# Optimization experiments

Measured on AMD Instinct MI355X. Metric: run time of the kernel, lower is better.

## Reference

```python
import jax, jax.numpy as jnp
import numpy as np

D_MODEL = 256
D_IN = (D_MODEL + 1) ** 2  # 66049


def setup_inputs() -> dict:
    key = jax.random.key(0)
    k1, k2, k3, k4 = jax.random.split(key, 4)
    X = jax.random.normal(k1, (16, 256, 256), dtype=jnp.float32)
    X_aux = jax.random.normal(k2, (16, 256, 256), dtype=jnp.float32)
    # nn.Linear params: weight [out, in], bias [out]
    W = jax.random.normal(k3, (D_MODEL, D_IN), dtype=jnp.float32) / np.sqrt(D_IN)
    b = jax.random.normal(k4, (D_MODEL,), dtype=jnp.float32) * 0.01
    return {"X": X, "X_aux": X_aux, "W": W, "b": b}


def reference(X, X_aux, W, b):
    bsz, t, d = X.shape
    ones = jnp.ones((bsz, t, 1), dtype=X.dtype)
    Xa = jnp.concatenate([ones, X], axis=2)        # [b, t, d+1]
    Xb = jnp.concatenate([ones, X_aux], axis=2)    # [b, t, d+1]
    # outer product per (b, t): [b, t, d+1, d+1]
    tf = jnp.einsum("bti,btj->btij", Xa, Xb)
    tf = tf.reshape(bsz, t, -1)                    # [b, t, (d+1)^2]
    out = jnp.einsum("btk,ok->bto", tf, W) + b     # [b, t, d_model]
    return out
```

## Files before the change

### kernel.cpp

```cpp
#include <hip/hip_runtime.h>
#include <hip/hip_bf16.h>


#define DI 66049

typedef __attribute__((ext_vector_type(8))) short bf16x8;
typedef __attribute__((ext_vector_type(4))) float f32x4;

__device__ __forceinline__ unsigned short f2b(float f) {
  union { __hip_bfloat16 h; unsigned short u; } cv;
  cv.h = __float2bfloat16(f);
  return cv.u;
}

__device__ __forceinline__ bf16x8 pack8(f32x4 lo, f32x4 hi) {
  bf16x8 r;
  r[0] = (short)f2b(lo[0]); r[1] = (short)f2b(lo[1]);
  r[2] = (short)f2b(lo[2]); r[3] = (short)f2b(lo[3]);
  r[4] = (short)f2b(hi[0]); r[5] = (short)f2b(hi[1]);
  r[6] = (short)f2b(hi[2]); r[7] = (short)f2b(hi[3]);
  return r;
}

__device__ __forceinline__ void gload16(const void* g, void* l) {
  __builtin_amdgcn_global_load_lds(
      (const __attribute__((address_space(1))) unsigned int*)g,
      (__attribute__((address_space(3))) unsigned int*)l, 16, 0, 0);
}

__global__ void prep_w(const float* __restrict__ W, unsigned short* __restrict__ Bp) {
  const int c = blockIdx.x;
  const int o = (blockIdx.y << 2) + (threadIdx.x >> 6);
  const int j = (threadIdx.x & 63) << 2;
  const float* wrow = W + (size_t)o * DI;
  float v0, v1, v2, v3;
  if (c < 256) {
    const int bse = (c + 1) * 257 + 1 + j;
    v0 = wrow[bse]; v1 = wrow[bse + 1]; v2 = wrow[bse + 2]; v3 = wrow[bse + 3];
  } else if (c == 256) {
    const int bse = 1 + j;
    v0 = wrow[bse]; v1 = wrow[bse + 1]; v2 = wrow[bse + 2]; v3 = wrow[bse + 3];
  } else {
    v0 = wrow[(j + 1) * 257]; v1 = wrow[(j + 2) * 257];
    v2 = wrow[(j + 3) * 257]; v3 = wrow[(j + 4) * 257];
  }
  unsigned short* dst = Bp + (((size_t)c << 8) + o) * 256 + j;
  const unsigned int lo = (unsigned int)f2b(v0) | ((unsigned int)f2b(v1) << 16);
  const unsigned int hi = (unsigned int)f2b(v2) | ((unsigned int)f2b(v3) << 16);
  *(uint2*)dst = make_uint2(lo, hi);
}

__global__ void prep_xt(const float* __restrict__ X, float* __restrict__ Xt) {
  __shared__ float t[32][33];
  const int tx = threadIdx.x, ty = threadIdx.y;
  const int bt0 = blockIdx.x << 5, c0 = blockIdx.y << 5;
#pragma unroll
  for (int k = 0; k < 4; ++k) {
    const int row = (ty << 2) + k;
    t[row][tx] = X[(size_t)(bt0 + row) * 256 + c0 + tx];
  }
  __syncthreads();
#pragma unroll
  for (int k = 0; k < 4; ++k) {
    const int row = (ty << 2) + k;
    Xt[(size_t)(c0 + row) * 4096 + bt0 + tx] = t[tx][row];
  }
}

#define PACK_AS(SRC)                                                           \
  {                                                                            \
    const int _row = tid >> 2, _q = tid & 3;                                   \
    const float* _rp = (SRC) + (size_t)(bt0 + _row) * 256 + (_q << 6);         \
    const int _sx = _row & 15;                                                 \
    _Pragma("unroll") for (int _w = 0; _w < 8; ++_w) {                         \
      f32x4 _lo = *(const f32x4*)(_rp + (_w << 3));                            \
      f32x4 _hi = *(const f32x4*)(_rp + (_w << 3) + 4);                        \
      const int _slot = (_q << 3) + _w;                                        \
      *(bf16x8*)(&As[_row * 256 + ((_slot ^ _sx) << 3)]) = pack8(_lo, _hi);    \
    }                                                                          \
  }

#define STAGE_U(V, SLOT)                                                       \
  {                                                                            \
    const unsigned short* _bse =                                               \
        Bp + ((size_t)(c0 + ((V) >> 3)) << 16) + (((V) & 7) << 5);             \
    gload16(_bse + stg_off0, &Bs[SLOT][(size_t)tid << 3]);                     \
    gload16(_bse + stg_off1, &Bs[SLOT][(size_t)(512 + tid) << 3]);             \
  }

#define READ_FRAGS(U, S)                                                       \
  {                                                                            \
    const int _uh4 = ((U) & 7) << 2;                                           \
    _Pragma("unroll") for (int _rg = 0; _rg < 4; ++_rg) {                      \
      const int _ra = wr + (_rg << 4) + l15;                                   \
      fa[S][_rg] = *(const bf16x8*)(&As[_ra * 256 +                            \
                                        (((_uh4 + lg) ^ (_ra & 15)) << 3)]);   \
    }                                                                          \
    _Pragma("unroll") for (int _fn = 0; _fn < 4; ++_fn) {                      \
      const int _rb = (wn << 6) + (_fn << 4) + l15;                            \
      fb[S][_fn] = *(const bf16x8*)(&Bs[(U) & 3][_rb * 32 +                    \
                                        ((lg ^ ((_rb >> 1) & 3)) << 3)]);      \
    }                                                                          \
  }

__global__ __launch_bounds__(512, 1) void gemm_r10(
    const float* __restrict__ X, const float* __restrict__ Xb,
    const float* __restrict__ Xt, const unsigned short* __restrict__ Bp,
    float* __restrict__ P) {
  __shared__ __align__(16) unsigned short As[128 * 256];
  __shared__ __align__(16) unsigned short Bs[4][256 * 32];
  __shared__ __align__(16) float Ss[33 * 128];

  const int tid = threadIdx.x;
  const int rid = blockIdx.x;

  int bx, c0, nCh, Pslice;
  const float* Asrc;
  if (rid < 256) {
    const int slice = rid & 7;
    bx = rid >> 3;
    c0 = slice << 5;
    nCh = (slice == 7) ? 33 : 32;
    Asrc = Xb;
    Pslice = slice;
  } else {
    bx = rid - 256;
    c0 = 257;
    nCh = 1;
    Asrc = X;
    Pslice = 8;
  }
  const int bt0 = bx << 7;
  const int nU = nCh << 3;

  const int wid = tid >> 6, lane = tid & 63;
  const int wm = wid >> 2, wn = wid & 3;
  const int wr = wm << 6;
  const int l15 = lane & 15, lg = lane >> 4;

  const int idx0 = tid, idx1 = 512 + tid;
  const int row0 = idx0 >> 2, row1 = idx1 >> 2;
  const unsigned stg_off0 =
      (unsigned)(row0 * 256 + (((idx0 & 3) ^ ((row0 >> 1) & 3)) << 3));
  const unsigned stg_off1 =
      (unsigned)(row1 * 256 + (((idx1 & 3) ^ ((row1 >> 1) & 3)) << 3));

  PACK_AS(Asrc);
  for (int i = tid; i < (nCh << 7); i += 512) {
    const int ci2 = i >> 7, r = i & 127;
    const int c = c0 + ci2;
    Ss[i] = (c < 256) ? Xt[(size_t)c * 4096 + bt0 + r] : 1.0f;
  }
  STAGE_U(0, 0);
  STAGE_U(1, 1);
  STAGE_U(2, 2);
  __syncthreads();

  bf16x8 fa[2][4], fb[2][4];
  READ_FRAGS(0, 0);

  f32x4 acc[4][4] = {};

  for (int ci = 0; ci < nCh; ++ci) {
    f32x4 t[4][4] = {};
    f32x4 s4[4];
#pragma unroll
    for (int uh = 0; uh < 8; ++uh) {
      const int u = (ci << 3) + uh;
      int v = u + 3;
      if (v > nU - 1) v = nU - 1;
      STAGE_U(v, (u + 3) & 3);
      asm volatile("s_waitcnt vmcnt(4)" ::: "memory");
      __builtin_amdgcn_s_barrier();
      int un = u + 1;
      if (un > nU - 1) un = nU - 1;
      if (uh & 1) {
        READ_FRAGS(un, 0);
      } else {
        READ_FRAGS(un, 1);
      }
      if (uh == 7) {
#pragma unroll
        for (int rg = 0; rg < 4; ++rg)
          s4[rg] =
              *(const f32x4*)(&Ss[(ci << 7) + wr + (rg << 4) + (lg << 2)]);
      }
      __builtin_amdgcn_s_setprio(1);
#pragma unroll
      for (int rg = 0; rg < 4; ++rg)
#pragma unroll
        for (int fn = 0; fn < 4; ++fn)
          t[rg][fn] = (uh & 1)
                          ? __builtin_amdgcn_mfma_f32_16x16x32_bf16(
                                fa[1][rg], fb[1][fn], t[rg][fn], 0, 0, 0)
                          : __builtin_amdgcn_mfma_f32_16x16x32_bf16(
                                fa[0][rg], fb[0][fn], t[rg][fn], 0, 0, 0);
      __builtin_amdgcn_s_setprio(0);
    }
#pragma unroll
    for (int rg = 0; rg < 4; ++rg)
#pragma unroll
      for (int fn = 0; fn < 4; ++fn) acc[rg][fn] += s4[rg] * t[rg][fn];
  }

  float* pp = P + ((size_t)Pslice << 20);
#pragma unroll
  for (int rg = 0; rg < 4; ++rg) {
    const int row = bt0 + wr + (rg << 4) + (lg << 2);
#pragma unroll
    for (int fn = 0; fn < 4; ++fn) {
      const int col = (wn << 6) + (fn << 4) + l15;
#pragma unroll
      for (int e = 0; e < 4; ++e)
        pp[(size_t)(row + e) * 256 + col] = acc[rg][fn][e];
    }
  }
}

__global__ void reduce_k(const float* __restrict__ P, const float* __restrict__ W,
                         const float* __restrict__ b, float* __restrict__ out,
                         int nsl) {
  const int idx = blockIdx.x * 256 + threadIdx.x;
  const int o = idx & 255;
  float v = b[o] + W[(size_t)o * DI];
  for (int s = 0; s < nsl; ++s) v += P[idx + (size_t)s * 1048576];
  out[idx] = v;
}

__global__ void init_k(const float* __restrict__ W, const float* __restrict__ b,
                       float* __restrict__ out) {
  const int idx = blockIdx.x * 256 + threadIdx.x;
  const int o = idx & 255;
  out[idx] = b[o] + W[(size_t)o * DI];
}

__global__ __launch_bounds__(256, 4) void gemm_fb(
    const float* __restrict__ X, const float* __restrict__ Xa,
    const float* __restrict__ W, float* __restrict__ Out) {
  __shared__ __align__(16) unsigned short Asf[128 * 64];
  __shared__ __align__(16) unsigned short Bsf[128 * 64];
  const int tid = threadIdx.x;
  const int bx = blockIdx.x, by = blockIdx.y, bz = blockIdx.z;
  const int S = gridDim.z;
  const int bt0 = bx << 7, o0 = by << 7;
  const int q = 258 / S, r = 258 % S;
  const int c0 = bz * q + (bz < r ? bz : r);
  const int ccnt = q + (bz < r ? 1 : 0);
  const int nK = ccnt << 2;
  const int wid = tid >> 6, lane = tid & 63;
  const int wr = (wid >> 1) << 6, wc = (wid & 1) << 6;
  const int ar = tid >> 1;
  const int ah = (tid & 1) << 5;
  const float* xrow = X + (size_t)(bt0 + ar) * 256;
  const float* varow = Xa + (size_t)(bt0 + ar) * 256;
  f32x4 acc[4][4] = {};
  for (int kt = 0; kt < nK; ++kt) {
    const int c = c0 + (kt >> 2);
    const int j0 = (kt & 3) << 6;
    __syncthreads();
    {
      const float* vs = (c == 257) ? xrow : varow;
      float s = 1.0f;
      if (c < 256) s = xrow[c];
      const f32x4* vp = (const f32x4*)(vs + j0 + ah);
      f32x4 v[8];
#pragma unroll
      for (int qq = 0; qq < 8; ++qq) v[qq] = vp[qq];
      unsigned short* aw = Asf + ar * 64;
      const int sl0 = ah >> 3, sx = ar & 7;
#pragma unroll
      for (int w = 0; w < 4; ++w) {
        bf16x8 pk;
#pragma unroll
        for (int e = 0; e < 8; ++e)
          pk[e] = (short)f2b(s * v[w * 2 + (e >> 2)][e & 3]);
        *(bf16x8*)(aw + (((sl0 + w) ^ sx) << 3)) = pk;
      }
    }
    {
      const int orow = tid >> 1;
      const int jh = (tid & 1) << 5;
      const float* wrow = W + (size_t)(o0 + orow) * DI;
      float tmp[32];
      if (c < 256) {
        const int bse = (c + 1) * 257 + 1 + j0 + jh;
#pragma unroll
        for (int i = 0; i < 32; ++i) tmp[i] = wrow[bse + i];
      } else if (c == 256) {
        const int bse = 1 + j0 + jh;
#pragma unroll
        for (int i = 0; i < 32; ++i) tmp[i] = wrow[bse + i];
      } else {
#pragma unroll
        for (int i = 0; i < 32; ++i) tmp[i] = wrow[(j0 + jh + i + 1) * 257];
      }
      unsigned short* bw = Bsf + orow * 64;
      const int sl0 = jh >> 3, sx = orow & 7;
#pragma unroll
      for (int w = 0; w < 4; ++w) {
        bf16x8 pk;
#pragma unroll
        for (int e = 0; e < 8; ++e) pk[e] = (short)f2b(tmp[w * 8 + e]);
        *(bf16x8*)(bw + (((sl0 + w) ^ sx) << 3)) = pk;
      }
    }
    __syncthreads();
#pragma unroll
    for (int kk = 0; kk < 2; ++kk) {
      const int kslot = (kk << 2) + (lane >> 4);
      bf16x8 af[4], bfr2[4];
#pragma unroll
      for (int fm = 0; fm < 4; ++fm) {
        const int row = wr + (fm << 4) + (lane & 15);
        af[fm] = *(const bf16x8*)(Asf + row * 64 + ((kslot ^ (row & 7)) << 3));
      }
#pragma unroll
      for (int fn = 0; fn < 4; ++fn) {
        const int row = wc + (fn << 4) + (lane & 15);
        bfr2[fn] = *(const bf16x8*)(Bsf + row * 64 + ((kslot ^ (row & 7)) << 3));
      }
#pragma unroll
      for (int fm = 0; fm < 4; ++fm)
#pragma unroll
        for (int fn = 0; fn < 4; ++fn)
          acc[fm][fn] = __builtin_amdgcn_mfma_f32_16x16x32_bf16(
              af[fm], bfr2[fn], acc[fm][fn], 0, 0, 0);
    }
  }
  const int r0 = (lane >> 4) << 2;
  const int cl = lane & 15;
#pragma unroll
  for (int fm = 0; fm < 4; ++fm) {
    const int row = bt0 + wr + (fm << 4) + r0;
#pragma unroll
    for (int fn = 0; fn < 4; ++fn) {
      const int col = o0 + wc + (fn << 4) + cl;
#pragma unroll
      for (int rr = 0; rr < 4; ++rr)
        atomicAdd(Out + (size_t)(row + rr) * 256 + col, acc[fm][fn][rr]);
    }
  }
}

extern "C" void kernel_launch(void* const* d_in, const int* in_sizes, int n_in,
                              void* d_out, int out_size, void* d_ws, size_t ws_size,
                              hipStream_t stream) {
  const float* X  = (const float*)d_in[0];
  const float* Xa = (const float*)d_in[1];
  const float* W  = (const float*)d_in[2];
  const float* b  = (const float*)d_in[3];
  float* out = (float*)d_out;

  const size_t WBF_SZ = (size_t)258 * 256 * 256 * 2;
  const size_t XT_SZ  = (size_t)256 * 4096 * 4;
  const size_t PART1  = (size_t)4096 * 256 * 4;

  if (ws_size >= WBF_SZ + XT_SZ + 9 * PART1) {
    unsigned short* Bp = (unsigned short*)d_ws;
    float* Xt = (float*)((char*)d_ws + WBF_SZ);
    float* P  = (float*)((char*)d_ws + WBF_SZ + XT_SZ);
    prep_w<<<dim3(258, 64), 256, 0, stream>>>(W, Bp);
    prep_xt<<<dim3(128, 8), dim3(32, 8), 0, stream>>>(X, Xt);
    gemm_r10<<<dim3(288), 512, 0, stream>>>(X, Xa, Xt, Bp, P);
    reduce_k<<<4096, 256, 0, stream>>>(P, W, b, out, 9);
  } else {
    init_k<<<4096, 256, 0, stream>>>(W, b, out);
    gemm_fb<<<dim3(32, 2, 4), 256, 0, stream>>>(X, Xa, W, out);
  }
}
```

Before: 174.3 us.

## Load B fragments directly from global into registers, dropping LDS staging and barriers

The GEMM kernel stops staging W tiles into a 4-slot LDS ring with global_load_lds and per-step barriers. Each wave now loads its B fragments straight from global memory into registers, one step ahead, with register double buffering. This removes the LDS traffic and workgroup barriers for B and frees LDS. In exchange, the four waves that share a column range each fetch the same B data separately, and global load latency is hidden only by a one-step prefetch.

```diff
diff --git a/kernel.cpp b/kernel.cpp
--- a/kernel.cpp
+++ b/kernel.cpp
@@ -6,6 +6,7 @@
 
 typedef __attribute__((ext_vector_type(8))) short bf16x8;
 typedef __attribute__((ext_vector_type(4))) float f32x4;
+typedef __attribute__((ext_vector_type(4))) int i32x4;
 
 __device__ __forceinline__ unsigned short f2b(float f) {
   union { __hip_bfloat16 h; unsigned short u; } cv;
@@ -20,12 +21,6 @@
   r[4] = (short)f2b(hi[0]); r[5] = (short)f2b(hi[1]);
   r[6] = (short)f2b(hi[2]); r[7] = (short)f2b(hi[3]);
   return r;
-}
-
-__device__ __forceinline__ void gload16(const void* g, void* l) {
-  __builtin_amdgcn_global_load_lds(
-      (const __attribute__((address_space(1))) unsigned int*)g,
-      (__attribute__((address_space(3))) unsigned int*)l, 16, 0, 0);
 }
 
 __global__ void prep_w(const float* __restrict__ W, unsigned short* __restrict__ Bp) {
@@ -80,35 +75,38 @@
     }                                                                          \
   }
 
-#define STAGE_U(V, SLOT)                                                       \
+#define READ_A(W, S)                                                           \
   {                                                                            \
-    const unsigned short* _bse =                                               \
-        Bp + ((size_t)(c0 + ((V) >> 3)) << 16) + (((V) & 7) << 5);             \
-    gload16(_bse + stg_off0, &Bs[SLOT][(size_t)tid << 3]);                     \
-    gload16(_bse + stg_off1, &Bs[SLOT][(size_t)(512 + tid) << 3]);             \
-  }
-
-#define READ_FRAGS(U, S)                                                       \
-  {                                                                            \
-    const int _uh4 = ((U) & 7) << 2;                                           \
     _Pragma("unroll") for (int _rg = 0; _rg < 4; ++_rg) {                      \
       const int _ra = wr + (_rg << 4) + l15;                                   \
       fa[S][_rg] = *(const bf16x8*)(&As[_ra * 256 +                            \
-                                        (((_uh4 + lg) ^ (_ra & 15)) << 3)]);   \
+                                        (((((W) << 2) + lg) ^ (_ra & 15))      \
+                                         << 3)]);                              \
     }                                                                          \
-    _Pragma("unroll") for (int _fn = 0; _fn < 4; ++_fn) {                      \
-      const int _rb = (wn << 6) + (_fn << 4) + l15;                            \
-      fb[S][_fn] = *(const bf16x8*)(&Bs[(U) & 3][_rb * 32 +                    \
-                                        ((lg ^ ((_rb >> 1) & 3)) << 3)]);      \
-    }                                                                          \
-  }
-
-__global__ __launch_bounds__(512, 1) void gemm_r10(
+  }
+
+#define ISSUE_B(S, UB)                                                         \
+  {                                                                            \
+    _Pragma("unroll") for (int _fn = 0; _fn < 4; ++_fn)                        \
+        fb[S][_fn] = *(const i32x4*)((UB) + boff[_fn]);                        \
+  }
+
+#define MFMA_SET(S)                                                            \
+  {                                                                            \
+    __builtin_amdgcn_s_setprio(1);                                             \
+    _Pragma("unroll") for (int _rg = 0; _rg < 4; ++_rg)                        \
+      _Pragma("unroll") for (int _fn = 0; _fn < 4; ++_fn)                      \
+        t[_rg][_fn] = __builtin_amdgcn_mfma_f32_16x16x32_bf16(                 \
+            fa[S][_rg], __builtin_bit_cast(bf16x8, fb[S][_fn]),                \
+            t[_rg][_fn], 0, 0, 0);                                             \
+    __builtin_amdgcn_s_setprio(0);                                             \
+  }
+
+__global__ __launch_bounds__(512, 1) void gemm_r14(
     const float* __restrict__ X, const float* __restrict__ Xb,
     const float* __restrict__ Xt, const unsigned short* __restrict__ Bp,
     float* __restrict__ P) {
   __shared__ __align__(16) unsigned short As[128 * 256];
-  __shared__ __align__(16) unsigned short Bs[4][256 * 32];
   __shared__ __align__(16) float Ss[33 * 128];
 
   const int tid = threadIdx.x;
@@ -138,12 +136,10 @@
   const int wr = wm << 6;
   const int l15 = lane & 15, lg = lane >> 4;
 
-  const int idx0 = tid, idx1 = 512 + tid;
-  const int row0 = idx0 >> 2, row1 = idx1 >> 2;
-  const unsigned stg_off0 =
-      (unsigned)(row0 * 256 + (((idx0 & 3) ^ ((row0 >> 1) & 3)) << 3));
-  const unsigned stg_off1 =
-      (unsigned)(row1 * 256 + (((idx1 & 3) ^ ((row1 >> 1) & 3)) << 3));
+  unsigned boff[4];
+#pragma unroll
+  for (int fn = 0; fn < 4; ++fn)
+    boff[fn] = (unsigned)(((wn << 6) + (fn << 4) + l15) * 256 + (lg << 3));
 
   PACK_AS(Asrc);
   for (int i = tid; i < (nCh << 7); i += 512) {
@@ -151,52 +147,34 @@
     const int c = c0 + ci2;
     Ss[i] = (c < 256) ? Xt[(size_t)c * 4096 + bt0 + r] : 1.0f;
   }
-  STAGE_U(0, 0);
-  STAGE_U(1, 1);
-  STAGE_U(2, 2);
   __syncthreads();
 
-  bf16x8 fa[2][4], fb[2][4];
-  READ_FRAGS(0, 0);
+  i32x4 fb[2][4];
+  bf16x8 fa[2][4];
+
+  ISSUE_B(0, Bp + ((size_t)c0 << 16));
+  READ_A(0, 0);
 
   f32x4 acc[4][4] = {};
 
   for (int ci = 0; ci < nCh; ++ci) {
     f32x4 t[4][4] = {};
+#pragma unroll
+    for (int uh = 0; uh < 8; ++uh) {
+      const int S = uh & 1, S2 = S ^ 1;
+      const int u = (ci << 3) + uh;
+      int v = u + 1;
+      if (v > nU - 1) v = nU - 1;
+      const unsigned short* ub =
+          Bp + ((size_t)(c0 + (v >> 3)) << 16) + ((v & 7) << 5);
+      ISSUE_B(S2, ub);
+      READ_A((uh + 1) & 7, S2);
+      MFMA_SET(S);
+    }
     f32x4 s4[4];
 #pragma unroll
-    for (int uh = 0; uh < 8; ++uh) {
-      const int u = (ci << 3) + uh;
-      int v = u + 3;
-      if (v > nU - 1) v = nU - 1;
-      STAGE_U(v, (u + 3) & 3);
-      asm volatile("s_waitcnt vmcnt(4)" ::: "memory");
-      __builtin_amdgcn_s_barrier();
-      int un = u + 1;
-      if (un > nU - 1) un = nU - 1;
-      if (uh & 1) {
-        READ_FRAGS(un, 0);
-      } else {
-        READ_FRAGS(un, 1);
-      }
-      if (uh == 7) {
-#pragma unroll
-        for (int rg = 0; rg < 4; ++rg)
-          s4[rg] =
-              *(const f32x4*)(&Ss[(ci << 7) + wr + (rg << 4) + (lg << 2)]);
-      }
-      __builtin_amdgcn_s_setprio(1);
-#pragma unroll
-      for (int rg = 0; rg < 4; ++rg)
-#pragma unroll
-        for (int fn = 0; fn < 4; ++fn)
-          t[rg][fn] = (uh & 1)
-                          ? __builtin_amdgcn_mfma_f32_16x16x32_bf16(
-                                fa[1][rg], fb[1][fn], t[rg][fn], 0, 0, 0)
-                          : __builtin_amdgcn_mfma_f32_16x16x32_bf16(
-                                fa[0][rg], fb[0][fn], t[rg][fn], 0, 0, 0);
-      __builtin_amdgcn_s_setprio(0);
-    }
+    for (int rg = 0; rg < 4; ++rg)
+      s4[rg] = *(const f32x4*)(&Ss[(ci << 7) + wr + (rg << 4) + (lg << 2)]);
 #pragma unroll
     for (int rg = 0; rg < 4; ++rg)
 #pragma unroll
@@ -361,7 +339,7 @@
     float* P  = (float*)((char*)d_ws + WBF_SZ + XT_SZ);
     prep_w<<<dim3(258, 64), 256, 0, stream>>>(W, Bp);
     prep_xt<<<dim3(128, 8), dim3(32, 8), 0, stream>>>(X, Xt);
-    gemm_r10<<<dim3(288), 512, 0, stream>>>(X, Xa, Xt, Bp, P);
+    gemm_r14<<<dim3(288), 512, 0, stream>>>(X, Xa, Xt, Bp, P);
     reduce_k<<<4096, 256, 0, stream>>>(P, W, b, out, 9);
   } else {
     init_k<<<4096, 256, 0, stream>>>(W, b, out);
```

After: 380.2 us. 2.18x slower.
